# Optimization experiments

Measured on AMD Instinct MI355X. Metric: run time of the kernel, lower is better.

The kernel has to match this reference:

```python
import jax, jax.numpy as jnp
import numpy as np

N = 50000          # number of rows / ego agents
A = 65             # num_agents + 1 (slot dimension)
DEG = 32           # neighbors per row
EMB = 32           # embedding_dim
HID = 16           # mlp hidden (mlp_pre_pool_dims = [32, 16, 32])
BOT = 32           # bottleneck_dim = h_dim
NEG_INF = -jnp.inf


def setup_inputs() -> dict:
    key = jax.random.key(0)
    ks = jax.random.split(key, 8)
    corr_index = jax.random.normal(ks[0], (N, A, 2), dtype=jnp.float32)
    lstm_state = jax.random.normal(ks[1], (N, BOT), dtype=jnp.float32)
    # edge list with unique (row, slot) pairs so scatter-set is well defined
    col0 = np.repeat(np.arange(N, dtype=np.int32), DEG)
    col2 = np.tile(np.arange(DEG, dtype=np.int32), N)
    col1 = np.random.default_rng(1).integers(0, A, size=N * DEG).astype(np.int32)
    nei_index = jnp.asarray(np.stack([col0, col1, col2], axis=1))  # [E,3]
    # parameters (Linear weights stored as [in, out])
    def lin(k, fin, fout):
        bound = 1.0 / np.sqrt(fin)
        kw, kb = jax.random.split(k)
        W = jax.random.uniform(kw, (fin, fout), jnp.float32, -bound, bound)
        b = jax.random.uniform(kb, (fout,), jnp.float32, -bound, bound)
        return W, b
    W_se, b_se = lin(ks[2], 2, EMB)
    W1, b1 = lin(ks[3], EMB, HID)
    W2, b2 = lin(ks[4], HID, BOT)
    return {"corr_index": corr_index, "nei_index": nei_index,
            "lstm_state": lstm_state, "W_se": W_se, "b_se": b_se,
            "W1": W1, "b1": b1, "W2": W2, "b2": b2}


def reference(corr_index, nei_index, lstm_state, W_se, b_se, W1, b1, W2, b2):
    # gather relative positions for each edge: [E, 2]
    rel = corr_index[nei_index[:, 0], nei_index[:, 1]]
    # spatial embedding + MLP (Linear+ReLU, Linear+ReLU)
    r_t = rel @ W_se + b_se                         # [E, EMB]
    h = jax.nn.relu(r_t @ W1 + b1)                  # [E, HID]
    h = jax.nn.relu(h @ W2 + b2)                    # [E, BOT]
    # scatter into dense -inf buffer, max over slot dim, zero out empty rows
    H = jnp.full((N, A, BOT), NEG_INF, dtype=h.dtype)
    H = H.at[nei_index[:, 0], nei_index[:, 2]].set(h, unique_indices=True)
    pool_h = jnp.max(H, axis=1)                     # [N, BOT]
    pool_h = jnp.where(jnp.isneginf(pool_h), 0.0, pool_h)
    return pool_h
```

## Files before the change

### kernel.cpp

```cpp
#include <hip/hip_runtime.h>

#define NODES 50000
#define NA    65
#define NDEG  32


__global__ __launch_bounds__(256, 1) void fused_kernel(
    const float* __restrict__ corr,
    const int*   __restrict__ nei,
    const float* __restrict__ W_se,
    const float* __restrict__ b_se,
    const float* __restrict__ W1,
    const float* __restrict__ b1,
    const float* __restrict__ W2,
    const float* __restrict__ b2,
    float* __restrict__ out)
{
    __shared__ __align__(16) float fold[48];
    int t = threadIdx.x;
    if (t < 48) {
        float s;
        if (t < 32) {
            int c = t >> 4, j = t & 15;
            s = 0.0f;
#pragma unroll
            for (int e = 0; e < 32; ++e)
                s = fmaf(W_se[c * 32 + e], W1[e * 16 + j], s);
        } else {
            int j = t - 32;
            s = b1[j];
#pragma unroll
            for (int e = 0; e < 32; ++e)
                s = fmaf(b_se[e], W1[e * 16 + j], s);
        }
        fold[t] = s;
    }
    __syncthreads();

    int tid = blockIdx.x * 256 + t;
    if (tid >= NODES * 8) return;
    int n  = tid >> 3;
    int k0 = (tid & 7) * 4;

    float Wc0[16], Wc1[16], bc[16];
    {
        const float4* fv = (const float4*)fold;
#pragma unroll
        for (int j = 0; j < 4; ++j) {
            float4 x = fv[j], y = fv[4 + j], z = fv[8 + j];
            Wc0[4*j] = x.x; Wc0[4*j+1] = x.y; Wc0[4*j+2] = x.z; Wc0[4*j+3] = x.w;
            Wc1[4*j] = y.x; Wc1[4*j+1] = y.y; Wc1[4*j+2] = y.z; Wc1[4*j+3] = y.w;
            bc[4*j]  = z.x; bc[4*j+1]  = z.y; bc[4*j+2]  = z.z; bc[4*j+3]  = z.w;
        }
    }

#define W2LD(i) float4 w2_##i = *(const float4*)(W2 + (i) * 32 + k0)
    W2LD(0);  W2LD(1);  W2LD(2);  W2LD(3);
    W2LD(4);  W2LD(5);  W2LD(6);  W2LD(7);
    W2LD(8);  W2LD(9);  W2LD(10); W2LD(11);
    W2LD(12); W2LD(13); W2LD(14); W2LD(15);
#undef W2LD
    float4 b2v = *(const float4*)(b2 + k0);

    float4 vmax = make_float4(0.0f, 0.0f, 0.0f, 0.0f);

    const float2* corrf = (const float2*)corr + (size_t)n * NA;
    const int*    neip  = nei + (size_t)n * (NDEG * 3) + 1;

#define L2ROW(i) do {                               \
        float hj = h1[i];                           \
        acc.x = fmaf(hj, w2_##i.x, acc.x);          \
        acc.y = fmaf(hj, w2_##i.y, acc.y);          \
        acc.z = fmaf(hj, w2_##i.z, acc.z);          \
        acc.w = fmaf(hj, w2_##i.w, acc.w);          \
    } while (0)

#define MLP_STEP(r0, r1) do {                                               \
        float h1[16];                                                       \
        _Pragma("unroll")                                                   \
        for (int j = 0; j < 16; ++j)                                        \
            h1[j] = fmaxf(0.0f, fmaf((r0), Wc0[j], fmaf((r1), Wc1[j], bc[j]))); \
        float4 acc = b2v;                                                   \
        L2ROW(0);  L2ROW(1);  L2ROW(2);  L2ROW(3);                          \
        L2ROW(4);  L2ROW(5);  L2ROW(6);  L2ROW(7);                          \
        L2ROW(8);  L2ROW(9);  L2ROW(10); L2ROW(11);                         \
        L2ROW(12); L2ROW(13); L2ROW(14); L2ROW(15);                         \
        vmax.x = fmaxf(vmax.x, acc.x);                                      \
        vmax.y = fmaxf(vmax.y, acc.y);                                      \
        vmax.z = fmaxf(vmax.z, acc.z);                                      \
        vmax.w = fmaxf(vmax.w, acc.w);                                      \
    } while (0)

    int aA[4], aB[4];
    float2 rA[4], rB[4];
#pragma unroll
    for (int u = 0; u < 4; ++u) aA[u] = neip[u * 3];
#pragma unroll
    for (int u = 0; u < 4; ++u) aB[u] = neip[(4 + u) * 3];
#pragma unroll
    for (int u = 0; u < 4; ++u) rA[u] = corrf[aA[u]];

#pragma unroll
    for (int c = 0; c < 8; c += 2) {
#pragma unroll
        for (int u = 0; u < 4; ++u) rB[u] = corrf[aB[u]];
        if (c + 2 < 8) {
#pragma unroll
            for (int u = 0; u < 4; ++u) aA[u] = neip[((c + 2) * 4 + u) * 3];
        }
#pragma unroll
        for (int u = 0; u < 4; ++u) MLP_STEP(rA[u].x, rA[u].y);

        if (c + 2 < 8) {
#pragma unroll
            for (int u = 0; u < 4; ++u) rA[u] = corrf[aA[u]];
        }
        if (c + 3 < 8) {
#pragma unroll
            for (int u = 0; u < 4; ++u) aB[u] = neip[((c + 3) * 4 + u) * 3];
        }
#pragma unroll
        for (int u = 0; u < 4; ++u) MLP_STEP(rB[u].x, rB[u].y);
    }
#undef MLP_STEP
#undef L2ROW

    *(float4*)(out + (size_t)n * 32 + k0) = vmax;
}

extern "C" void kernel_launch(void* const* d_in, const int* in_sizes, int n_in,
                              void* d_out, int out_size, void* d_ws, size_t ws_size,
                              hipStream_t stream) {
    const float* corr = (const float*)d_in[0];
    const int*   nei  = (const int*)d_in[1];
    const float* W_se = (const float*)d_in[3];
    const float* b_se = (const float*)d_in[4];
    const float* W1   = (const float*)d_in[5];
    const float* b1   = (const float*)d_in[6];
    const float* W2   = (const float*)d_in[7];
    const float* b2   = (const float*)d_in[8];
    float* out = (float*)d_out;

    int total  = NODES * 8;
    int blocks = (total + 255) / 256;
    hipLaunchKernelGGL(fused_kernel, dim3(blocks), dim3(256), 0, stream,
                       corr, nei, W_se, b_se, W1, b1, W2, b2, out);
}
```

Measured before the change: 129.8 us.

## Stage gathered edge positions in shared memory and use packed FP32 math

Each block now stages the gathered relative positions for its 32 nodes into LDS, using cooperative coalesced reads of the neighbor-index column followed by one corr gather per edge. The per-thread prefetch pipeline, in which all 8 threads of a node redundantly gathered the same 32 edges, is removed. The MLP math is rewritten with two-wide packed FMA/max vectors, and the second layer splits its reduction across the two vector lanes before a final add. This trims redundant global gathers and halves the ALU instruction count, at the cost of a block-wide barrier before compute and some extra LDS use.

After: 127.8 us. About the same (-1.6%).

```diff
diff --git a/kernel.cpp b/kernel.cpp
--- a/kernel.cpp
+++ b/kernel.cpp
@@ -4,6 +4,17 @@
 #define NA    65
 #define NDEG  32
 
+
+typedef float v2f __attribute__((ext_vector_type(2)));
+
+static __device__ __forceinline__ v2f pk_fma(v2f a, v2f b, v2f c) {
+    return __builtin_elementwise_fma(a, b, c);
+}
+static __device__ __forceinline__ v2f pk_max(v2f a, v2f b) {
+    return __builtin_elementwise_max(a, b);
+}
+
+#define RELSTRIDE 34
 
 __global__ __launch_bounds__(256, 1) void fused_kernel(
     const float* __restrict__ corr,
@@ -16,8 +27,12 @@
     const float* __restrict__ b2,
     float* __restrict__ out)
 {
-    __shared__ __align__(16) float fold[48];
-    int t = threadIdx.x;
+    __shared__ __align__(16) float  fold[48];
+    __shared__ __align__(16) float2 relbuf[32 * RELSTRIDE];
+
+    int t  = threadIdx.x;
+    int nb = blockIdx.x * 32;
+
     if (t < 48) {
         float s;
         if (t < 32) {
@@ -35,97 +50,80 @@
         }
         fold[t] = s;
     }
+
+#pragma unroll
+    for (int u = 0; u < 4; ++u) {
+        int g    = t + 256 * u;
+        int nl   = g >> 5;
+        int d    = g & 31;
+        int node = nb + nl;
+        if (node < NODES) {
+            int idx = nei[((size_t)node * NDEG + d) * 3 + 1];
+            relbuf[nl * RELSTRIDE + d] =
+                ((const float2*)corr)[(size_t)node * NA + idx];
+        }
+    }
     __syncthreads();
 
-    int tid = blockIdx.x * 256 + t;
-    if (tid >= NODES * 8) return;
-    int n  = tid >> 3;
-    int k0 = (tid & 7) * 4;
+    int nl   = t >> 3;
+    int node = nb + nl;
+    int k0   = (t & 7) * 4;
+    if (node >= NODES) return;
 
-    float Wc0[16], Wc1[16], bc[16];
+    v2f wc0v[8], wc1v[8], bcv[8];
     {
-        const float4* fv = (const float4*)fold;
+        const v2f* fv = (const v2f*)fold;
 #pragma unroll
-        for (int j = 0; j < 4; ++j) {
-            float4 x = fv[j], y = fv[4 + j], z = fv[8 + j];
-            Wc0[4*j] = x.x; Wc0[4*j+1] = x.y; Wc0[4*j+2] = x.z; Wc0[4*j+3] = x.w;
-            Wc1[4*j] = y.x; Wc1[4*j+1] = y.y; Wc1[4*j+2] = y.z; Wc1[4*j+3] = y.w;
-            bc[4*j]  = z.x; bc[4*j+1]  = z.y; bc[4*j+2]  = z.z; bc[4*j+3]  = z.w;
+        for (int j = 0; j < 8; ++j) {
+            wc0v[j] = fv[j];
+            wc1v[j] = fv[8 + j];
+            bcv[j]  = fv[16 + j];
         }
     }
 
-#define W2LD(i) float4 w2_##i = *(const float4*)(W2 + (i) * 32 + k0)
-    W2LD(0);  W2LD(1);  W2LD(2);  W2LD(3);
-    W2LD(4);  W2LD(5);  W2LD(6);  W2LD(7);
-    W2LD(8);  W2LD(9);  W2LD(10); W2LD(11);
-    W2LD(12); W2LD(13); W2LD(14); W2LD(15);
-#undef W2LD
+#define W2T(p)                                                              \
+    float4 ra_##p = *(const float4*)(W2 + (2 * (p)) * 32 + k0);             \
+    float4 rb_##p = *(const float4*)(W2 + (2 * (p) + 1) * 32 + k0);         \
+    v2f w2_##p##_0 = {ra_##p.x, rb_##p.x};                                  \
+    v2f w2_##p##_1 = {ra_##p.y, rb_##p.y};                                  \
+    v2f w2_##p##_2 = {ra_##p.z, rb_##p.z};                                  \
+    v2f w2_##p##_3 = {ra_##p.w, rb_##p.w};
+    W2T(0) W2T(1) W2T(2) W2T(3) W2T(4) W2T(5) W2T(6) W2T(7)
+#undef W2T
+
     float4 b2v = *(const float4*)(b2 + k0);
 
-    float4 vmax = make_float4(0.0f, 0.0f, 0.0f, 0.0f);
+    float vm0 = 0.0f, vm1 = 0.0f, vm2 = 0.0f, vm3 = 0.0f;
 
-    const float2* corrf = (const float2*)corr + (size_t)n * NA;
-    const int*    neip  = nei + (size_t)n * (NDEG * 3) + 1;
+    const float2* rp = relbuf + nl * RELSTRIDE;
 
-#define L2ROW(i) do {                               \
-        float hj = h1[i];                           \
-        acc.x = fmaf(hj, w2_##i.x, acc.x);          \
-        acc.y = fmaf(hj, w2_##i.y, acc.y);          \
-        acc.z = fmaf(hj, w2_##i.z, acc.z);          \
-        acc.w = fmaf(hj, w2_##i.w, acc.w);          \
+#define L2P(p) do {                                                         \
+        acc0 = pk_fma(h1v[p], w2_##p##_0, acc0);                            \
+        acc1 = pk_fma(h1v[p], w2_##p##_1, acc1);                            \
+        acc2 = pk_fma(h1v[p], w2_##p##_2, acc2);                            \
+        acc3 = pk_fma(h1v[p], w2_##p##_3, acc3);                            \
     } while (0)
 
-#define MLP_STEP(r0, r1) do {                                               \
-        float h1[16];                                                       \
-        _Pragma("unroll")                                                   \
-        for (int j = 0; j < 16; ++j)                                        \
-            h1[j] = fmaxf(0.0f, fmaf((r0), Wc0[j], fmaf((r1), Wc1[j], bc[j]))); \
-        float4 acc = b2v;                                                   \
-        L2ROW(0);  L2ROW(1);  L2ROW(2);  L2ROW(3);                          \
-        L2ROW(4);  L2ROW(5);  L2ROW(6);  L2ROW(7);                          \
-        L2ROW(8);  L2ROW(9);  L2ROW(10); L2ROW(11);                         \
-        L2ROW(12); L2ROW(13); L2ROW(14); L2ROW(15);                         \
-        vmax.x = fmaxf(vmax.x, acc.x);                                      \
-        vmax.y = fmaxf(vmax.y, acc.y);                                      \
-        vmax.z = fmaxf(vmax.z, acc.z);                                      \
-        vmax.w = fmaxf(vmax.w, acc.w);                                      \
-    } while (0)
+#pragma unroll
+    for (int d = 0; d < NDEG; ++d) {
+        float2 r = rp[d];
+        v2f r0s = {r.x, r.x}, r1s = {r.y, r.y};
+        v2f h1v[8];
+#pragma unroll
+        for (int j = 0; j < 8; ++j)
+            h1v[j] = pk_max((v2f)(0.0f),
+                     pk_fma(r0s, wc0v[j], pk_fma(r1s, wc1v[j], bcv[j])));
+        v2f acc0 = {b2v.x, 0.0f}, acc1 = {b2v.y, 0.0f};
+        v2f acc2 = {b2v.z, 0.0f}, acc3 = {b2v.w, 0.0f};
+        L2P(0); L2P(1); L2P(2); L2P(3); L2P(4); L2P(5); L2P(6); L2P(7);
+        vm0 = fmaxf(vm0, acc0.x + acc0.y);
+        vm1 = fmaxf(vm1, acc1.x + acc1.y);
+        vm2 = fmaxf(vm2, acc2.x + acc2.y);
+        vm3 = fmaxf(vm3, acc3.x + acc3.y);
+    }
+#undef L2P
 
-    int aA[4], aB[4];
-    float2 rA[4], rB[4];
-#pragma unroll
-    for (int u = 0; u < 4; ++u) aA[u] = neip[u * 3];
-#pragma unroll
-    for (int u = 0; u < 4; ++u) aB[u] = neip[(4 + u) * 3];
-#pragma unroll
-    for (int u = 0; u < 4; ++u) rA[u] = corrf[aA[u]];
-
-#pragma unroll
-    for (int c = 0; c < 8; c += 2) {
-#pragma unroll
-        for (int u = 0; u < 4; ++u) rB[u] = corrf[aB[u]];
-        if (c + 2 < 8) {
-#pragma unroll
-            for (int u = 0; u < 4; ++u) aA[u] = neip[((c + 2) * 4 + u) * 3];
-        }
-#pragma unroll
-        for (int u = 0; u < 4; ++u) MLP_STEP(rA[u].x, rA[u].y);
-
-        if (c + 2 < 8) {
-#pragma unroll
-            for (int u = 0; u < 4; ++u) rA[u] = corrf[aA[u]];
-        }
-        if (c + 3 < 8) {
-#pragma unroll
-            for (int u = 0; u < 4; ++u) aB[u] = neip[((c + 3) * 4 + u) * 3];
-        }
-#pragma unroll
-        for (int u = 0; u < 4; ++u) MLP_STEP(rB[u].x, rB[u].y);
-    }
-#undef MLP_STEP
-#undef L2ROW
-
-    *(float4*)(out + (size_t)n * 32 + k0) = vmax;
+    *(float4*)(out + (size_t)node * 32 + k0) = make_float4(vm0, vm1, vm2, vm3);
 }
 
 extern "C" void kernel_launch(void* const* d_in, const int* in_sizes, int n_in,
@@ -141,8 +139,7 @@
     const float* b2   = (const float*)d_in[8];
     float* out = (float*)d_out;
 
-    int total  = NODES * 8;
-    int blocks = (total + 255) / 256;
+    int blocks = (NODES + 31) / 32;
     hipLaunchKernelGGL(fused_kernel, dim3(blocks), dim3(256), 0, stream,
                        corr, nei, W_se, b_se, W1, b1, W2, b2, out);
 }
```
